# Kernel tuning notes

Hardware: AMD Instinct MI355X
Metric: run time of the kernel (lower is better)

Reference implementation:

```python
import jax, jax.numpy as jnp
import numpy as np

N_NODES = 100000
N_EDGES = 3200000


def gcn_conv(x, W, b, src, dst, n_nodes):
    # x: [N, Fin] -> [N, Fout]; PyG GCNConv: linear, add self-loops,
    # symmetric norm D^-1/2 A_hat D^-1/2, sum-aggregate over incoming edges, + bias
    h = x @ W  # [N, Fout]
    loop = jnp.arange(n_nodes, dtype=src.dtype)
    src2 = jnp.concatenate([src, loop])
    dst2 = jnp.concatenate([dst, loop])
    deg = jax.ops.segment_sum(jnp.ones_like(dst2, dtype=h.dtype), dst2, num_segments=n_nodes)
    dinv = jnp.where(deg > 0, jax.lax.rsqrt(deg), 0.0)
    norm = dinv[src2] * dinv[dst2]  # [E+N]
    msgs = h[src2] * norm[:, None]  # gather + scale
    out = jax.ops.segment_sum(msgs, dst2, num_segments=n_nodes)  # scatter-add
    return out + b


def setup_inputs() -> dict:
    key = jax.random.key(0)
    k1, k2, k3, k4 = jax.random.split(key, 4)
    x = jax.random.normal(k1, (N_NODES, 16), dtype=jnp.float32)
    edge_index = jax.random.randint(k2, (2, N_EDGES), 0, N_NODES, dtype=jnp.int64)
    W1 = jax.random.normal(k3, (16, 32), dtype=jnp.float32) * (1.0 / np.sqrt(16))
    b1 = jnp.zeros((32,), dtype=jnp.float32)
    W2 = jax.random.normal(k4, (32, 3), dtype=jnp.float32) * (1.0 / np.sqrt(32))
    b2 = jnp.zeros((3,), dtype=jnp.float32)
    return {"x": x, "edge_index": edge_index, "W1": W1, "b1": b1, "W2": W2, "b2": b2}


def reference(x, edge_index, W1, b1, W2, b2):
    src, dst = edge_index[0], edge_index[1]
    n = x.shape[0]
    h = gcn_conv(x, W1, b1, src, dst, n)
    h = jax.nn.relu(h)
    h = gcn_conv(h, W2, b2, src, dst, n)
    return jax.nn.log_softmax(h, axis=1)
```

## Files before the change

kernel.cpp:

```cpp
#include <hip/hip_runtime.h>
#include <math.h>


#define NN 100000
#define NE 3200000
#define BSH 7
#define NPB 128
#define NB  ((NN + NPB - 1) / NPB)
#define EPB 12544
#define CAP 6144
#define SCAP 5632

__device__ __forceinline__ float bl(unsigned u) { return __uint_as_float(u << 16); }
__device__ __forceinline__ float bh(unsigned u) { return __uint_as_float(u & 0xFFFF0000u); }
__device__ __forceinline__ unsigned rne(float f) {
    unsigned u = __float_as_uint(f);
    return (u + 0x7FFFu + ((u >> 16) & 1u)) >> 16;
}

typedef int vint4 __attribute__((ext_vector_type(4)));


__global__ void __launch_bounds__(256) k_zero(int* __restrict__ bcur) {
    int t = blockIdx.x * 256 + threadIdx.x;
    if (t < NB) bcur[t] = 0;
}

__global__ void __launch_bounds__(1024) k_partition(
        const int* __restrict__ src, const int* __restrict__ dst,
        int* __restrict__ bcur, unsigned int* __restrict__ ebuf, int E) {
    __shared__ int hist[NB];
    __shared__ int lbase[NB];
    __shared__ int gbase[NB];
    __shared__ int lcur[NB];
    __shared__ unsigned int sebuf[EPB];
    __shared__ unsigned short sbkt[EPB];
    __shared__ int wsum[16];
    int tid = threadIdx.x;
    int e0 = blockIdx.x * EPB;
    int e1 = min(e0 + EPB, E);
    int cnt = e1 - e0;
    int cnt4 = cnt >> 2;
    if (tid < NB) { hist[tid] = 0; lcur[tid] = 0; }
    __syncthreads();
    const vint4* d4 = (const vint4*)(dst + e0);
    vint4 dc[4];
#pragma unroll
    for (int r = 0; r < 4; r++) {
        int i4 = r * 1024 + tid;
        if (i4 < cnt4) {
            dc[r] = d4[i4];
            atomicAdd(&hist[dc[r].x >> BSH], 1);
            atomicAdd(&hist[dc[r].y >> BSH], 1);
            atomicAdd(&hist[dc[r].z >> BSH], 1);
            atomicAdd(&hist[dc[r].w >> BSH], 1);
        }
    }
    __syncthreads();
    int lane = tid & 63, w = tid >> 6;
    {
        int v = (tid < NB) ? hist[tid] : 0;
        int incl = v;
#pragma unroll
        for (int off = 1; off < 64; off <<= 1) {
            int u = __shfl_up(incl, off);
            if (lane >= off) incl += u;
        }
        if (lane == 63) wsum[w] = incl;
        __syncthreads();
        int woff = 0;
#pragma unroll
        for (int k = 0; k < 16; k++) woff += (k < w) ? wsum[k] : 0;
        int excl = incl - v + woff;
        if (tid < NB) {
            lbase[tid] = excl;
            gbase[tid] = tid * CAP + (v ? atomicAdd(&bcur[tid], v) : 0);
        }
        __syncthreads();
    }
    const vint4* s4 = (const vint4*)(src + e0);
#pragma unroll
    for (int r = 0; r < 4; r++) {
        int i4 = r * 1024 + tid;
        if (i4 < cnt4) {
            vint4 sv = s4[i4];
            int d, b, p;
            d = dc[r].x; b = d >> BSH; p = lbase[b] + atomicAdd(&lcur[b], 1);
            sebuf[p] = (unsigned)sv.x | ((unsigned)(d & (NPB - 1)) << 20);
            sbkt[p] = (unsigned short)b;
            d = dc[r].y; b = d >> BSH; p = lbase[b] + atomicAdd(&lcur[b], 1);
            sebuf[p] = (unsigned)sv.y | ((unsigned)(d & (NPB - 1)) << 20);
            sbkt[p] = (unsigned short)b;
            d = dc[r].z; b = d >> BSH; p = lbase[b] + atomicAdd(&lcur[b], 1);
            sebuf[p] = (unsigned)sv.z | ((unsigned)(d & (NPB - 1)) << 20);
            sbkt[p] = (unsigned short)b;
            d = dc[r].w; b = d >> BSH; p = lbase[b] + atomicAdd(&lcur[b], 1);
            sebuf[p] = (unsigned)sv.w | ((unsigned)(d & (NPB - 1)) << 20);
            sbkt[p] = (unsigned short)b;
        }
    }
    __syncthreads();
    for (int p = tid; p < cnt; p += 1024) {
        int b = sbkt[p];
        ebuf[gbase[b] + (p - lbase[b])] = sebuf[p];
    }
}

__global__ void __launch_bounds__(256) k_B(
        const unsigned int* __restrict__ ebuf, const int* __restrict__ bcur,
        const float* __restrict__ x, int* __restrict__ deg,
        unsigned int* __restrict__ xsb, int N) {
    __shared__ int hist[NPB];
    int b = blockIdx.x, tid = threadIdx.x;
    int beg = b * CAP, cnt = bcur[b];
    if (tid < NPB) hist[tid] = 0;
    __syncthreads();
    for (int j = tid; j < cnt; j += 256)
        atomicAdd(&hist[ebuf[beg + j] >> 20], 1);
    __syncthreads();
    if (tid < NPB) {
        int node = b * NPB + tid;
        if (node < N) {
            int v = hist[tid];
            deg[node] = v;
            float di = rsqrtf((float)(v + 1));
            const float4* x4 = (const float4*)(x + (size_t)node * 16);
            float4 A = x4[0], Bv = x4[1], Cv = x4[2], Dv = x4[3];
            uint4 o0, o1;
            o0.x = rne(A.x * di) | (rne(A.y * di) << 16);
            o0.y = rne(A.z * di) | (rne(A.w * di) << 16);
            o0.z = rne(Bv.x * di) | (rne(Bv.y * di) << 16);
            o0.w = rne(Bv.z * di) | (rne(Bv.w * di) << 16);
            o1.x = rne(Cv.x * di) | (rne(Cv.y * di) << 16);
            o1.y = rne(Cv.z * di) | (rne(Cv.w * di) << 16);
            o1.z = rne(Dv.x * di) | (rne(Dv.y * di) << 16);
            o1.w = rne(Dv.z * di) | (rne(Dv.w * di) << 16);
            uint4* op = (uint4*)xsb;
            op[(size_t)node * 2 + 0] = o0;
            op[(size_t)node * 2 + 1] = o1;
        }
    }
}

__global__ void __launch_bounds__(512) k_L1(
        const unsigned int* __restrict__ ebuf, const int* __restrict__ bcur,
        const int* __restrict__ deg, const unsigned int* __restrict__ xsb,
        const float* __restrict__ W1, const float* __restrict__ b1,
        const float* __restrict__ W2, unsigned int* __restrict__ g2b, int N) {
    __shared__ int scol[SCAP];
    __shared__ float sacc[NPB][17];
    __shared__ int sdeg[NPB];
    __shared__ int base[NPB];
    __shared__ int lcur[NPB];
    __shared__ float sdinv[NPB];
    __shared__ float W1s[512];
    __shared__ float W2s[96];
    __shared__ float b1s[32];
    __shared__ int wsum[2];
    int b = blockIdx.x, tid = threadIdx.x;
    int beg = b * CAP;
    int cnt = bcur[b];
    int cl = min(cnt, SCAP);
    W1s[tid < 512 ? tid : 0] = W1[tid < 512 ? tid : 0];
    if (tid < 96) W2s[tid] = W2[tid];
    if (tid < 32) b1s[tid] = b1[tid];
    int lane = tid & 63, w = tid >> 6;
    int v = 0;
    if (tid < NPB) {
        int node = b * NPB + tid;
        v = (node < N) ? deg[node] : 0;
        sdeg[tid] = v;
        lcur[tid] = 0;
        sdinv[tid] = rsqrtf((float)(v + 1));
    }
    int incl = v;
#pragma unroll
    for (int off = 1; off < 64; off <<= 1) {
        int u = __shfl_up(incl, off);
        if (lane >= off) incl += u;
    }
    if (tid < NPB && lane == 63) wsum[w] = incl;
    __syncthreads();
    if (tid < NPB) base[tid] = incl - v + ((w == 1) ? wsum[0] : 0);
    __syncthreads();
    for (int j = tid; j < cl; j += 512) {
        unsigned pe = ebuf[beg + j];
        int dl = (int)(pe >> 20);
        int pos = base[dl] + atomicAdd(&lcur[dl], 1);
        if (pos < SCAP) scol[pos] = (int)(pe & 0xFFFFF);
    }
    __syncthreads();
    {
        int g = tid >> 4;
        int lq = tid & 15;
        int r = lq >> 1, c = lq & 1;
        const uint4* xb = (const uint4*)xsb;
#pragma unroll
        for (int p = 0; p < 4; p++) {
            int nib = p * 32 + g;
            int jb = base[nib];
            int je = jb + sdeg[nib];
            float a0 = 0.f, a1 = 0.f, a2 = 0.f, a3 = 0.f;
            float a4 = 0.f, a5 = 0.f, a6 = 0.f, a7 = 0.f;
            int j = jb + r;
            while (j + 8 < je) {
                int s0 = scol[j], s1 = scol[j + 8];
                uint4 q0 = xb[(size_t)s0 * 2 + c];
                uint4 q1 = xb[(size_t)s1 * 2 + c];
                a0 += bl(q0.x); a1 += bh(q0.x); a2 += bl(q0.y); a3 += bh(q0.y);
                a4 += bl(q0.z); a5 += bh(q0.z); a6 += bl(q0.w); a7 += bh(q0.w);
                a0 += bl(q1.x); a1 += bh(q1.x); a2 += bl(q1.y); a3 += bh(q1.y);
                a4 += bl(q1.z); a5 += bh(q1.z); a6 += bl(q1.w); a7 += bh(q1.w);
                j += 16;
            }
            if (j < je) {
                int s = scol[j];
                uint4 qq = xb[(size_t)s * 2 + c];
                a0 += bl(qq.x); a1 += bh(qq.x); a2 += bl(qq.y); a3 += bh(qq.y);
                a4 += bl(qq.z); a5 += bh(qq.z); a6 += bl(qq.w); a7 += bh(qq.w);
            }
#pragma unroll
            for (int off = 8; off >= 2; off >>= 1) {
                a0 += __shfl_down(a0, off);
                a1 += __shfl_down(a1, off);
                a2 += __shfl_down(a2, off);
                a3 += __shfl_down(a3, off);
                a4 += __shfl_down(a4, off);
                a5 += __shfl_down(a5, off);
                a6 += __shfl_down(a6, off);
                a7 += __shfl_down(a7, off);
            }
            if (lq < 2) {
                sacc[nib][c * 8 + 0] = a0; sacc[nib][c * 8 + 1] = a1;
                sacc[nib][c * 8 + 2] = a2; sacc[nib][c * 8 + 3] = a3;
                sacc[nib][c * 8 + 4] = a4; sacc[nib][c * 8 + 5] = a5;
                sacc[nib][c * 8 + 6] = a6; sacc[nib][c * 8 + 7] = a7;
            }
        }
    }
    __syncthreads();
    if (tid < NPB) {
        int node = b * NPB + tid;
        if (node < N) {
            float di = sdinv[tid];
            const uint4* xb = (const uint4*)xsb;
            uint4 s0 = xb[(size_t)node * 2], s1 = xb[(size_t)node * 2 + 1];
            float a[16] = {
                sacc[tid][0] + bl(s0.x),  sacc[tid][1] + bh(s0.x),
                sacc[tid][2] + bl(s0.y),  sacc[tid][3] + bh(s0.y),
                sacc[tid][4] + bl(s0.z),  sacc[tid][5] + bh(s0.z),
                sacc[tid][6] + bl(s0.w),  sacc[tid][7] + bh(s0.w),
                sacc[tid][8] + bl(s1.x),  sacc[tid][9] + bh(s1.x),
                sacc[tid][10] + bl(s1.y), sacc[tid][11] + bh(s1.y),
                sacc[tid][12] + bl(s1.z), sacc[tid][13] + bh(s1.z),
                sacc[tid][14] + bl(s1.w), sacc[tid][15] + bh(s1.w)};
            float p0 = 0.f, p1 = 0.f, p2 = 0.f;
#pragma unroll
            for (int jj = 0; jj < 32; jj++) {
                float o = 0.f;
#pragma unroll
                for (int k = 0; k < 16; k++) o = fmaf(a[k], W1s[k * 32 + jj], o);
                float z = fmaxf(fmaf(di, o, b1s[jj]), 0.f);
                p0 = fmaf(z, W2s[jj * 3 + 0], p0);
                p1 = fmaf(z, W2s[jj * 3 + 1], p1);
                p2 = fmaf(z, W2s[jj * 3 + 2], p2);
            }
            uint2 o;
            o.x = rne(p0 * di) | (rne(p1 * di) << 16);
            o.y = rne(p2 * di);
            ((uint2*)g2b)[node] = o;
        }
    }
}

__global__ void __launch_bounds__(512) k_L2(
        const unsigned int* __restrict__ ebuf, const int* __restrict__ bcur,
        const int* __restrict__ deg, const unsigned int* __restrict__ g2b,
        const float* __restrict__ b2, float* __restrict__ out, int N) {
    __shared__ int scol[SCAP];
    __shared__ int sdeg[NPB];
    __shared__ int base[NPB];
    __shared__ int lcur[NPB];
    __shared__ float sdinv[NPB];
    __shared__ int wsum[2];
    int b = blockIdx.x, tid = threadIdx.x;
    int beg = b * CAP;
    int cnt = bcur[b];
    int cl = min(cnt, SCAP);
    int lane = tid & 63, w = tid >> 6;
    int v = 0;
    if (tid < NPB) {
        int node = b * NPB + tid;
        v = (node < N) ? deg[node] : 0;
        sdeg[tid] = v;
        lcur[tid] = 0;
        sdinv[tid] = rsqrtf((float)(v + 1));
    }
    int incl = v;
#pragma unroll
    for (int off = 1; off < 64; off <<= 1) {
        int u = __shfl_up(incl, off);
        if (lane >= off) incl += u;
    }
    if (tid < NPB && lane == 63) wsum[w] = incl;
    __syncthreads();
    if (tid < NPB) base[tid] = incl - v + ((w == 1) ? wsum[0] : 0);
    __syncthreads();
    for (int j = tid; j < cl; j += 512) {
        unsigned pe = __builtin_nontemporal_load(&ebuf[beg + j]);
        int dl = (int)(pe >> 20);
        int pos = base[dl] + atomicAdd(&lcur[dl], 1);
        if (pos < SCAP) scol[pos] = (int)(pe & 0xFFFFF);
    }
    __syncthreads();
    {
        int lo = tid & 7;
        const uint2* gb = (const uint2*)g2b;
#pragma unroll
        for (int p = 0; p < 2; p++) {
            int nib = p * 64 + (tid >> 3);
            int node = b * NPB + nib;
            int jb = base[nib];
            int je = jb + sdeg[nib];
            float a0 = 0.f, a1 = 0.f, a2 = 0.f;
            int j = jb + lo;
            while (j + 8 < je) {
                uint2 v0 = gb[scol[j]];
                uint2 v1 = gb[scol[j + 8]];
                a0 += bl(v0.x); a1 += bh(v0.x); a2 += bl(v0.y);
                a0 += bl(v1.x); a1 += bh(v1.x); a2 += bl(v1.y);
                j += 16;
            }
            if (j < je) {
                uint2 vv = gb[scol[j]];
                a0 += bl(vv.x); a1 += bh(vv.x); a2 += bl(vv.y);
            }
#pragma unroll
            for (int off = 4; off >= 1; off >>= 1) {
                a0 += __shfl_down(a0, off);
                a1 += __shfl_down(a1, off);
                a2 += __shfl_down(a2, off);
            }
            if (lo == 0 && node < N) {
                float di = sdinv[nib];
                uint2 sv = gb[node];
                float v0 = fmaf(di, a0 + bl(sv.x), b2[0]);
                float v1 = fmaf(di, a1 + bh(sv.x), b2[1]);
                float v2 = fmaf(di, a2 + bl(sv.y), b2[2]);
                float m = fmaxf(v0, fmaxf(v1, v2));
                float lse = m + logf(expf(v0 - m) + expf(v1 - m) + expf(v2 - m));
                out[(size_t)node * 3 + 0] = v0 - lse;
                out[(size_t)node * 3 + 1] = v1 - lse;
                out[(size_t)node * 3 + 2] = v2 - lse;
            }
        }
    }
}


extern "C" void kernel_launch(void* const* d_in, const int* in_sizes, int n_in,
                              void* d_out, int out_size, void* d_ws, size_t ws_size,
                              hipStream_t stream) {
    const float* x  = (const float*)d_in[0];
    const int*   ei = (const int*)d_in[1];
    const float* W1 = (const float*)d_in[2];
    const float* b1 = (const float*)d_in[3];
    const float* W2 = (const float*)d_in[4];
    const float* b2 = (const float*)d_in[5];
    float* out = (float*)d_out;

    const int* src = ei;
    const int* dst = ei + NE;

    unsigned int* ebuf = (unsigned int*)d_ws;
    unsigned int* xsb  = ebuf + (size_t)NB * CAP;
    unsigned int* g2b  = xsb + (size_t)NN * 8;
    int*          deg  = (int*)(g2b + (size_t)NN * 2);
    int*          bcur = deg + NN;

    const int B = 256;
    int gbP = (NE + EPB - 1) / EPB;
    int gbZ = (NB + B - 1) / B;

    k_zero<<<gbZ, B, 0, stream>>>(bcur);
    k_partition<<<gbP, 1024, 0, stream>>>(src, dst, bcur, ebuf, NE);
    k_B<<<NB, B, 0, stream>>>(ebuf, bcur, x, deg, xsb, NN);
    k_L1<<<NB, 512, 0, stream>>>(ebuf, bcur, deg, xsb, W1, b1, W2, g2b, NN);
    k_L2<<<NB, 512, 0, stream>>>(ebuf, bcur, deg, g2b, b2, out, NN);
}
```

Before: 88.48 us.

## Split each destination bucket across two half-blocks in both aggregation kernels

```diff
diff --git a/kernel.cpp b/kernel.cpp
--- a/kernel.cpp
+++ b/kernel.cpp
@@ -6,10 +6,11 @@
 #define NE 3200000
 #define BSH 7
 #define NPB 128
+#define HNPB 64
 #define NB  ((NN + NPB - 1) / NPB)
 #define EPB 12544
 #define CAP 6144
-#define SCAP 5632
+#define HSCAP 2816
 
 __device__ __forceinline__ float bl(unsigned u) { return __uint_as_float(u << 16); }
 __device__ __forceinline__ float bh(unsigned u) { return __uint_as_float(u & 0xFFFF0000u); }
@@ -142,52 +143,54 @@
     }
 }
 
-__global__ void __launch_bounds__(512) k_L1(
+__global__ void __launch_bounds__(256) k_L1(
         const unsigned int* __restrict__ ebuf, const int* __restrict__ bcur,
         const int* __restrict__ deg, const unsigned int* __restrict__ xsb,
         const float* __restrict__ W1, const float* __restrict__ b1,
         const float* __restrict__ W2, unsigned int* __restrict__ g2b, int N) {
-    __shared__ int scol[SCAP];
-    __shared__ float sacc[NPB][17];
-    __shared__ int sdeg[NPB];
-    __shared__ int base[NPB];
-    __shared__ int lcur[NPB];
-    __shared__ float sdinv[NPB];
+    __shared__ int scol[HSCAP];
+    __shared__ float sacc[HNPB][17];
+    __shared__ int sdeg[HNPB];
+    __shared__ int base[HNPB];
+    __shared__ int lcur[HNPB];
+    __shared__ float sdinv[HNPB];
     __shared__ float W1s[512];
     __shared__ float W2s[96];
     __shared__ float b1s[32];
-    __shared__ int wsum[2];
-    int b = blockIdx.x, tid = threadIdx.x;
+    int bb = blockIdx.x, tid = threadIdx.x;
+    int b = bb >> 1, half = bb & 1;
     int beg = b * CAP;
     int cnt = bcur[b];
-    int cl = min(cnt, SCAP);
-    W1s[tid < 512 ? tid : 0] = W1[tid < 512 ? tid : 0];
+    int nodebase = b * NPB + half * HNPB;
+    for (int t = tid; t < 512; t += 256) W1s[t] = W1[t];
     if (tid < 96) W2s[tid] = W2[tid];
     if (tid < 32) b1s[tid] = b1[tid];
-    int lane = tid & 63, w = tid >> 6;
     int v = 0;
-    if (tid < NPB) {
-        int node = b * NPB + tid;
+    if (tid < HNPB) {
+        int node = nodebase + tid;
         v = (node < N) ? deg[node] : 0;
         sdeg[tid] = v;
         lcur[tid] = 0;
         sdinv[tid] = rsqrtf((float)(v + 1));
     }
+    int lane = tid & 63;
     int incl = v;
 #pragma unroll
     for (int off = 1; off < 64; off <<= 1) {
         int u = __shfl_up(incl, off);
         if (lane >= off) incl += u;
     }
-    if (tid < NPB && lane == 63) wsum[w] = incl;
-    __syncthreads();
-    if (tid < NPB) base[tid] = incl - v + ((w == 1) ? wsum[0] : 0);
-    __syncthreads();
-    for (int j = tid; j < cl; j += 512) {
+    if (tid < HNPB) base[tid] = incl - v;
+    __syncthreads();
+    int dhi = half << 6;
+    for (int j = tid; j < cnt; j += 256) {
         unsigned pe = ebuf[beg + j];
         int dl = (int)(pe >> 20);
-        int pos = base[dl] + atomicAdd(&lcur[dl], 1);
-        if (pos < SCAP) scol[pos] = (int)(pe & 0xFFFFF);
+        if ((dl & 64) == dhi) {
+            int d6 = dl & 63;
+            int pos = base[d6] + atomicAdd(&lcur[d6], 1);
+            if (pos < HSCAP) scol[pos] = (int)(pe & 0xFFFFF);
+        }
     }
     __syncthreads();
     {
@@ -197,7 +200,7 @@
         const uint4* xb = (const uint4*)xsb;
 #pragma unroll
         for (int p = 0; p < 4; p++) {
-            int nib = p * 32 + g;
+            int nib = p * 16 + g;
             int jb = base[nib];
             int je = jb + sdeg[nib];
             float a0 = 0.f, a1 = 0.f, a2 = 0.f, a3 = 0.f;
@@ -239,8 +242,8 @@
         }
     }
     __syncthreads();
-    if (tid < NPB) {
-        int node = b * NPB + tid;
+    if (tid < HNPB) {
+        int node = nodebase + tid;
         if (node < N) {
             float di = sdinv[tid];
             const uint4* xb = (const uint4*)xsb;
@@ -273,44 +276,46 @@
     }
 }
 
-__global__ void __launch_bounds__(512) k_L2(
+__global__ void __launch_bounds__(256) k_L2(
         const unsigned int* __restrict__ ebuf, const int* __restrict__ bcur,
         const int* __restrict__ deg, const unsigned int* __restrict__ g2b,
         const float* __restrict__ b2, float* __restrict__ out, int N) {
-    __shared__ int scol[SCAP];
-    __shared__ int sdeg[NPB];
-    __shared__ int base[NPB];
-    __shared__ int lcur[NPB];
-    __shared__ float sdinv[NPB];
-    __shared__ int wsum[2];
-    int b = blockIdx.x, tid = threadIdx.x;
+    __shared__ int scol[HSCAP];
+    __shared__ int sdeg[HNPB];
+    __shared__ int base[HNPB];
+    __shared__ int lcur[HNPB];
+    __shared__ float sdinv[HNPB];
+    int bb = blockIdx.x, tid = threadIdx.x;
+    int b = bb >> 1, half = bb & 1;
     int beg = b * CAP;
     int cnt = bcur[b];
-    int cl = min(cnt, SCAP);
-    int lane = tid & 63, w = tid >> 6;
+    int nodebase = b * NPB + half * HNPB;
     int v = 0;
-    if (tid < NPB) {
-        int node = b * NPB + tid;
+    if (tid < HNPB) {
+        int node = nodebase + tid;
         v = (node < N) ? deg[node] : 0;
         sdeg[tid] = v;
         lcur[tid] = 0;
         sdinv[tid] = rsqrtf((float)(v + 1));
     }
+    int lane = tid & 63;
     int incl = v;
 #pragma unroll
     for (int off = 1; off < 64; off <<= 1) {
         int u = __shfl_up(incl, off);
         if (lane >= off) incl += u;
     }
-    if (tid < NPB && lane == 63) wsum[w] = incl;
-    __syncthreads();
-    if (tid < NPB) base[tid] = incl - v + ((w == 1) ? wsum[0] : 0);
-    __syncthreads();
-    for (int j = tid; j < cl; j += 512) {
-        unsigned pe = __builtin_nontemporal_load(&ebuf[beg + j]);
+    if (tid < HNPB) base[tid] = incl - v;
+    __syncthreads();
+    int dhi = half << 6;
+    for (int j = tid; j < cnt; j += 256) {
+        unsigned pe = ebuf[beg + j];
         int dl = (int)(pe >> 20);
-        int pos = base[dl] + atomicAdd(&lcur[dl], 1);
-        if (pos < SCAP) scol[pos] = (int)(pe & 0xFFFFF);
+        if ((dl & 64) == dhi) {
+            int d6 = dl & 63;
+            int pos = base[d6] + atomicAdd(&lcur[d6], 1);
+            if (pos < HSCAP) scol[pos] = (int)(pe & 0xFFFFF);
+        }
     }
     __syncthreads();
     {
@@ -318,8 +323,8 @@
         const uint2* gb = (const uint2*)g2b;
 #pragma unroll
         for (int p = 0; p < 2; p++) {
-            int nib = p * 64 + (tid >> 3);
-            int node = b * NPB + nib;
+            int nib = p * 32 + (tid >> 3);
+            int node = nodebase + nib;
             int jb = base[nib];
             int je = jb + sdeg[nib];
             float a0 = 0.f, a1 = 0.f, a2 = 0.f;
@@ -385,6 +390,6 @@
     k_zero<<<gbZ, B, 0, stream>>>(bcur);
     k_partition<<<gbP, 1024, 0, stream>>>(src, dst, bcur, ebuf, NE);
     k_B<<<NB, B, 0, stream>>>(ebuf, bcur, x, deg, xsb, NN);
-    k_L1<<<NB, 512, 0, stream>>>(ebuf, bcur, deg, xsb, W1, b1, W2, g2b, NN);
-    k_L2<<<NB, 512, 0, stream>>>(ebuf, bcur, deg, g2b, b2, out, NN);
-}
+    k_L1<<<NB * 2, B, 0, stream>>>(ebuf, bcur, deg, xsb, W1, b1, W2, g2b, NN);
+    k_L2<<<NB * 2, B, 0, stream>>>(ebuf, bcur, deg, g2b, b2, out, NN);
+}
```

Measured after the change: 94.76 us. +7.1%, slower.
